# Performance work log

Hardware: AMD Instinct MI355X
Metric: run time of the kernel (lower is better)

## Reference

```python
import jax, jax.numpy as jnp
import numpy as np

HIDDEN = 4096
N_HEADS = 32
N_KV_HEADS = 8
HEAD_DIM = HIDDEN // N_HEADS  # 128
N_GROUPS = N_HEADS // N_KV_HEADS  # 4
MAX_POS = 4096
B, S = 2, 2048


def _rope_tables(max_pos, dim):
    # Mirrors create_sinusoidal_positions: freqs [pos, dim/2] -> emb [pos, dim]
    freqs = np.einsum('i,j->ij', np.arange(max_pos),
                      1.0 / 10000 ** (np.arange(0, dim, 2) / dim)).astype('float32')
    emb = np.concatenate((freqs, freqs), axis=-1)  # [pos, dim]
    return jnp.asarray(np.sin(emb)), jnp.asarray(np.cos(emb))

_SIN, _COS = _rope_tables(MAX_POS, HEAD_DIM)


def _apply_rope(t, sin_pos, cos_pos):
    # t: [B,S,H,hd]; sin/cos: [B,S,1,hd]
    half = t.shape[-1] // 2
    rot = jnp.concatenate((-t[..., half:], t[..., :half]), axis=-1)
    return t * cos_pos + rot * sin_pos


def setup_inputs() -> dict:
    key = jax.random.key(0)
    ks = jax.random.split(key, 5)
    std = 0.02
    hidden_states = jax.random.normal(ks[0], (B, S, HIDDEN), dtype=jnp.float32)
    attention_mask = jnp.ones((B, S), dtype=jnp.float32)
    position_ids = jnp.broadcast_to(jnp.arange(S, dtype=jnp.int32)[None, :], (B, S))
    Wq = jax.random.normal(ks[1], (HIDDEN, N_HEADS * HEAD_DIM), dtype=jnp.float32) * std
    Wk = jax.random.normal(ks[2], (HIDDEN, N_KV_HEADS * HEAD_DIM), dtype=jnp.float32) * std
    Wv = jax.random.normal(ks[3], (HIDDEN, N_KV_HEADS * HEAD_DIM), dtype=jnp.float32) * std
    Wo = jax.random.normal(ks[4], (HIDDEN, HIDDEN), dtype=jnp.float32) * std
    return {'hidden_states': hidden_states, 'attention_mask': attention_mask,
            'position_ids': position_ids, 'Wq': Wq, 'Wk': Wk, 'Wv': Wv, 'Wo': Wo}


def reference(hidden_states, attention_mask, position_ids, Wq, Wk, Wv, Wo):
    b, s, _ = hidden_states.shape
    # QKV projections (no bias) + head split
    q = (hidden_states @ Wq).reshape(b, s, N_HEADS, HEAD_DIM)
    k = (hidden_states @ Wk).reshape(b, s, N_KV_HEADS, HEAD_DIM)
    v = (hidden_states @ Wv).reshape(b, s, N_KV_HEADS, HEAD_DIM)
    # Rotary embedding
    sin_pos = _SIN[position_ids][:, :, None, :]  # [B,S,1,hd]
    cos_pos = _COS[position_ids][:, :, None, :]
    q = _apply_rope(q, sin_pos, cos_pos)
    k = _apply_rope(k, sin_pos, cos_pos)
    # Repeat KV heads for grouped-query attention
    k = jnp.repeat(k, N_GROUPS, axis=2)  # [B,S,H,hd]
    v = jnp.repeat(v, N_GROUPS, axis=2)
    # Causal mask & padding mask -> additive bias
    causal = jnp.tril(jnp.ones((s, s), dtype=bool))[None, None]  # [1,1,S,S]
    pad = (attention_mask > 0)[:, None, None, :]                 # [B,1,1,S]
    mask = jnp.logical_and(causal, pad)
    neg = jnp.finfo(jnp.float32).min
    bias = jnp.where(mask, 0.0, neg).astype(jnp.float32)
    # Scaled dot-product attention (softmax in fp32, matching flax)
    scale = 1.0 / jnp.sqrt(jnp.asarray(HEAD_DIM, dtype=jnp.float32))
    scores = jnp.einsum('bqhd,bkhd->bhqk', q * scale, k) + bias
    attn = jax.nn.softmax(scores, axis=-1)
    out = jnp.einsum('bhqk,bkhd->bqhd', attn, v).reshape(b, s, HIDDEN)
    return out @ Wo
```

## Files before the change

kernel.cpp:

```cpp
#include <hip/hip_runtime.h>

typedef unsigned short u16;
typedef __attribute__((ext_vector_type(8))) short bf16x8;
typedef __attribute__((ext_vector_type(8))) unsigned short u16x8;
typedef __attribute__((ext_vector_type(4))) float f32x4;

#define HIDDEN 4096
#define NH 32
#define NKV 8
#define HD 128
#define BB 2
#define SS 2048
#define TOK (BB * SS)
#define MAXPOS 4096
#define NQKV 6144

__device__ __forceinline__ u16 f2bf(float f) {
  unsigned u = __float_as_uint(f);
  u += 0x7FFFu + ((u >> 16) & 1u);
  return (u16)(u >> 16);
}
__device__ __forceinline__ float bf2f(u16 u) {
  return __uint_as_float(((unsigned)u) << 16);
}

__device__ __forceinline__ void gload_lds16(const u16* g, u16* l) {
  __builtin_amdgcn_global_load_lds(
      (const __attribute__((address_space(1))) unsigned int*)g,
      (__attribute__((address_space(3))) unsigned int*)l, 16, 0, 0);
}

__device__ __forceinline__ u16* swzp(u16* base, int row, int col, int stride) {
  int off = (row * stride + col) * 2;
  off ^= (row & 7) << 4;
  return (u16*)((char*)base + off);
}
__device__ __forceinline__ const u16* swzc(const u16* base, int row, int col, int stride) {
  int off = (row * stride + col) * 2;
  off ^= (row & 7) << 4;
  return (const u16*)((const char*)base + off);
}


__global__ void conv_bf16(const float* __restrict__ X, u16* __restrict__ Y, int n8) {
  int i = blockIdx.x * 256 + threadIdx.x;
  if (i >= n8) return;
  const float4* p = (const float4*)X;
  float4 a = p[2 * (long)i], b = p[2 * (long)i + 1];
  u16x8 o;
  o[0] = f2bf(a.x); o[1] = f2bf(a.y); o[2] = f2bf(a.z); o[3] = f2bf(a.w);
  o[4] = f2bf(b.x); o[5] = f2bf(b.y); o[6] = f2bf(b.z); o[7] = f2bf(b.w);
  *(u16x8*)&Y[(long)i * 8] = o;
}

__global__ __launch_bounds__(256) void conv_transpose(const float* __restrict__ W,
                                                      u16* __restrict__ Wt,
                                                      int K, int N) {
  __shared__ float tile[64][65];
  const int n0 = blockIdx.x * 64, k0 = blockIdx.y * 64;
  const int t = threadIdx.x;
  const int r = t >> 4, c4 = (t & 15) * 4;
#pragma unroll
  for (int i = 0; i < 4; i++) {
    float4 v = *(const float4*)&W[(long)(k0 + r + i * 16) * N + n0 + c4];
    tile[r + i * 16][c4 + 0] = v.x;
    tile[r + i * 16][c4 + 1] = v.y;
    tile[r + i * 16][c4 + 2] = v.z;
    tile[r + i * 16][c4 + 3] = v.w;
  }
  __syncthreads();
#pragma unroll
  for (int i = 0; i < 4; i++) {
    int n = r + i * 16;
    ushort4 o;
    o.x = f2bf(tile[c4 + 0][n]);
    o.y = f2bf(tile[c4 + 1][n]);
    o.z = f2bf(tile[c4 + 2][n]);
    o.w = f2bf(tile[c4 + 3][n]);
    *(ushort4*)&Wt[(long)(n0 + n) * K + k0 + c4] = o;
  }
}


__global__ void rope_table(float* __restrict__ st, float* __restrict__ ct) {
  int i = blockIdx.x * 256 + threadIdx.x;
  int pos = i >> 6, j = i & 63;
  float inv = exp2f(-(float)(2 * j) * (13.287712379549449f / 128.f));
  float a = (float)pos * inv;
  st[i] = sinf(a);
  ct[i] = cosf(a);
}

__global__ void rope_apply(u16* __restrict__ T, const int* __restrict__ pid,
                           const float* __restrict__ st, const float* __restrict__ ct,
                           int nh, int total, float scale) {
  int i = blockIdx.x * 256 + threadIdx.x;
  if (i >= total) return;
  int j = i & 63;
  int rest = i >> 6;
  int h = rest % nh;
  int tok = rest / nh;
  int pos = pid[tok];
  long base = ((long)tok * nh + h) * 128;
  float c = ct[pos * 64 + j], s = st[pos * 64 + j];
  float a = bf2f(T[base + j]), b = bf2f(T[base + 64 + j]);
  T[base + j]      = f2bf((a * c - b * s) * scale);
  T[base + 64 + j] = f2bf((b * c + a * s) * scale);
}

__global__ void mask_flags(const float* __restrict__ amask, int* __restrict__ mf) {
  int i = threadIdx.x;
  if (i >= BB * (SS / 64)) return;
  int b = i / (SS / 64), tt = i % (SS / 64);
  int any = 0;
  for (int k = 0; k < 64; k++) any |= (amask[b * SS + tt * 64 + k] <= 0.f) ? 1 : 0;
  mf[i] = any;
}

__global__ __launch_bounds__(256) void vtrans(const u16* __restrict__ V, u16* __restrict__ Vt) {
  __shared__ u16 tile[64][68];
  const int s0 = blockIdx.x * 64, d0 = blockIdx.y * 64;
  const int bk = blockIdx.z;
  const int b = bk >> 3, kvh = bk & 7;
  const int t = threadIdx.x;
  const int r = t >> 4, c4 = (t & 15) * 4;
#pragma unroll
  for (int i = 0; i < 4; i++) {
    int s = s0 + r + i * 16;
    ushort4 v = *(const ushort4*)&V[(((long)b * SS + s) * NKV + kvh) * HD + d0 + c4];
    tile[r + i * 16][c4 + 0] = v.x;
    tile[r + i * 16][c4 + 1] = v.y;
    tile[r + i * 16][c4 + 2] = v.z;
    tile[r + i * 16][c4 + 3] = v.w;
  }
  __syncthreads();
#pragma unroll
  for (int i = 0; i < 4; i++) {
    int d = r + i * 16;
    ushort4 o;
    o.x = tile[c4 + 0][d];
    o.y = tile[c4 + 1][d];
    o.z = tile[c4 + 2][d];
    o.w = tile[c4 + 3][d];
    *(ushort4*)&Vt[(((long)bk) * HD + d0 + d) * SS + s0 + c4] = o;
  }
}


#define GEMM256_CORE(Aptr, Btptr, Kd)                                              \
  __shared__ __align__(16) u16 ring[65536];       \
  const int tid = threadIdx.x;                                                     \
  const int lane = tid & 63;                                                       \
  const int wid = tid >> 6;                                                        \
  const int wm = wid >> 2, wn = wid & 3;                                           \
  const int fr = lane & 15, fq = lane >> 4;                                        \
  const int sr = tid >> 2;                                 \
  const int ss = (tid & 3) ^ ((sr ^ (sr >> 2)) & 3);        \
  const int csl = (fq ^ ((fr ^ (fr >> 2)) & 3)) << 4;      \
  const u16* Ag0 = (Aptr) + (brow + sr) * (long)(Kd) + ss * 8;                     \
  const u16* Bg0 = (Btptr) + (bcol + sr) * (long)(Kd) + ss * 8;                    \
  f32x4 acc[8][4] = {};                                                            \
  auto stage = [&](int tt) {                                                       \
    u16* as_ = &ring[(tt & 3) * 16384];                                            \
    const u16* ag = Ag0 + (long)tt * 32;                                           \
    const u16* bg = Bg0 + (long)tt * 32;                                           \
    gload_lds16(ag, as_ + tid * 8);                                                \
    gload_lds16(ag + 128 * (long)(Kd), as_ + 4096 + tid * 8);                      \
    gload_lds16(bg, as_ + 8192 + tid * 8);                                         \
    gload_lds16(bg + 128 * (long)(Kd), as_ + 12288 + tid * 8);                     \
  };                                                                               \
  const int NT = (Kd) / 32;                                                        \
  stage(0); stage(1); stage(2);                                                    \
  _Pragma("unroll 1")                                                              \
  for (int t = 0; t < NT; ++t) {                                                   \
    if (t + 2 < NT)      asm volatile("s_waitcnt vmcnt(8)" ::: "memory");          \
    else if (t + 1 < NT) asm volatile("s_waitcnt vmcnt(4)" ::: "memory");          \
    else                 asm volatile("s_waitcnt vmcnt(0)" ::: "memory");          \
    __builtin_amdgcn_s_barrier();                                                  \
    __builtin_amdgcn_sched_barrier(0);                                             \
    if (t + 3 < NT) stage(t + 3);      \
    const u16* as_ = &ring[(t & 3) * 16384];                                       \
    bf16x8 af[8], bfv[4];                                                          \
    _Pragma("unroll") for (int m = 0; m < 8; m++)                                  \
      af[m] = *(const bf16x8*)((const char*)as_ +                                  \
                               ((wm * 128 + m * 16 + fr) << 6) + csl);             \
    _Pragma("unroll") for (int n = 0; n < 4; n++)                                  \
      bfv[n] = *(const bf16x8*)((const char*)as_ + 16384 +                         \
                                ((wn * 64 + n * 16 + fr) << 6) + csl);             \
    asm volatile("s_waitcnt lgkmcnt(0)" ::: "memory");                             \
    __builtin_amdgcn_sched_barrier(0);                                             \
    __builtin_amdgcn_s_setprio(1);                                                 \
    _Pragma("unroll") for (int m = 0; m < 8; m++)                                  \
      _Pragma("unroll") for (int n = 0; n < 4; n++)                                \
        acc[m][n] = __builtin_amdgcn_mfma_f32_16x16x32_bf16(af[m], bfv[n],         \
                                                            acc[m][n], 0, 0, 0);   \
    __builtin_amdgcn_s_setprio(0);                                                 \
  }

#define XCD_BLOCK_MAP()                                                            \
  const int nwg = gridDim.x * gridDim.y;                                           \
  int bid = blockIdx.y * gridDim.x + blockIdx.x;                                   \
  bid = (bid & 7) * (nwg >> 3) + (bid >> 3);                                       \
  const long brow = (long)(bid / gridDim.x) * 256;                                 \
  const long bcol = (long)(bid % gridDim.x) * 256;

__global__ __launch_bounds__(512) void gemm_qkv(const u16* __restrict__ A,
                                                const u16* __restrict__ Bt,
                                                u16* __restrict__ Qb,
                                                u16* __restrict__ Kb,
                                                u16* __restrict__ Vb) {
  XCD_BLOCK_MAP()
  GEMM256_CORE(A, Bt, HIDDEN)
  u16* dst;
  long nst, cb;
  if (bcol < 4096)      { dst = Qb; nst = 4096; cb = bcol; }
  else if (bcol < 5120) { dst = Kb; nst = 1024; cb = bcol - 4096; }
  else                  { dst = Vb; nst = 1024; cb = bcol - 5120; }
#pragma unroll
  for (int m = 0; m < 8; m++)
#pragma unroll
    for (int j = 0; j < 4; j++) {
      long row = brow + wm * 128 + m * 16 + fq * 4 + j;
#pragma unroll
      for (int n = 0; n < 4; n++)
        dst[row * nst + cb + wn * 64 + n * 16 + fr] = f2bf(acc[m][n][j]);
    }
}

__global__ __launch_bounds__(512) void gemm_out(const u16* __restrict__ A,
                                                const u16* __restrict__ Bt,
                                                float* __restrict__ C) {
  XCD_BLOCK_MAP()
  GEMM256_CORE(A, Bt, HIDDEN)
#pragma unroll
  for (int m = 0; m < 8; m++)
#pragma unroll
    for (int j = 0; j < 4; j++) {
      long row = brow + wm * 128 + m * 16 + fq * 4 + j;
#pragma unroll
      for (int n = 0; n < 4; n++)
        C[row * HIDDEN + bcol + wn * 64 + n * 16 + fr] = acc[m][n][j];
    }
}


__global__ __launch_bounds__(256) void attn_fwd(const u16* __restrict__ Q,
                                                const u16* __restrict__ K,
                                                const u16* __restrict__ Vt,
                                                const float* __restrict__ amask,
                                                const int* __restrict__ mflag,
                                                u16* __restrict__ O) {
  const int b = blockIdx.z, h = blockIdx.y;
  const int qi = gridDim.x - 1 - blockIdx.x;
  const int qb = qi * 64;
  const int kvh = h >> 2;
  const int t = threadIdx.x, lane = t & 63, w = t >> 6;
  const int fr = lane & 15, fq = lane >> 4;

  __shared__ u16 Kl[2][64 * 128];
  __shared__ u16 Vl[2][128 * 64];
  __shared__ u16 PlA[4][16 * 64];

  const int qrow = qb + w * 16 + fr;
  bf16x8 qf[4];
  {
    const long qbase = (((long)b * SS + qrow) * NH + h) * HD;
#pragma unroll
    for (int kk = 0; kk < 4; kk++)
      qf[kk] = *(const bf16x8*)&Q[qbase + kk * 32 + fq * 8];
  }

  const u16* Kh = K + (long)b * SS * NKV * HD + (long)kvh * HD;
  const u16* Vh = Vt + ((long)b * NKV + kvh) * (long)HD * SS;
  const float* Mh = amask + (long)b * SS;
  const int* Mf = mflag + b * (SS / 64);
  u16* Plw = PlA[w];

  int koff[4], voff[4];
#pragma unroll
  for (int i = 0; i < 4; i++) {
    int o = i * 4096 + t * 16;
    int rk = o >> 8;
    int ck = (o & 255) ^ ((rk & 7) << 4);
    koff[i] = rk * (NKV * HD) + (ck >> 1);
    int rv = o >> 7;
    int cv = (o & 127) ^ ((rv & 7) << 4);
    voff[i] = rv * SS + (cv >> 1);
  }
  auto stage = [&](int kv0, int buf) {
    const u16* Kt = Kh + (long)kv0 * (NKV * HD);
    const u16* Vs = Vh + kv0;
#pragma unroll
    for (int i = 0; i < 4; i++)
      gload_lds16(Kt + koff[i], &Kl[buf][i * 2048 + t * 8]);
#pragma unroll
    for (int i = 0; i < 4; i++)
      gload_lds16(Vs + voff[i], &Vl[buf][i * 2048 + t * 8]);
  };

  f32x4 oacc[8] = {};
  float mrow = -1e30f, lrow = 0.f;
  const float L2E = 1.4426950408889634f;
  const int nt = qi + 1;

  stage(0, 0);

  for (int kvt = 0; kvt < nt; kvt++) {
    const int cur = kvt & 1;
    const int kv0 = kvt * 64;

    __syncthreads();
    if (kvt + 1 < nt) stage(kv0 + 64, cur ^ 1);
    __builtin_amdgcn_sched_barrier(0);

    f32x4 sacc[4] = {};
    __builtin_amdgcn_s_setprio(1);
#pragma unroll
    for (int n = 0; n < 4; n++)
#pragma unroll
      for (int kk = 0; kk < 4; kk++) {
        bf16x8 kf = *(const bf16x8*)swzc(&Kl[cur][0], n * 16 + fr, kk * 32 + fq * 8, 128);
        sacc[n] = __builtin_amdgcn_mfma_f32_16x16x32_bf16(kf, qf[kk], sacc[n], 0, 0, 0);
      }
    __builtin_amdgcn_s_setprio(0);

    if (kvt == qi) {
#pragma unroll
      for (int n = 0; n < 4; n++)
#pragma unroll
        for (int j = 0; j < 4; j++) {
          const int key = kv0 + n * 16 + fq * 4 + j;
          if (key > qrow) sacc[n][j] = -1e30f;
        }
    }
    if (Mf[kvt]) {
#pragma unroll
      for (int n = 0; n < 4; n++) {
        float4 mkv = *(const float4*)&Mh[kv0 + n * 16 + fq * 4];
#pragma unroll
        for (int j = 0; j < 4; j++)
          if ((&mkv.x)[j] <= 0.f) sacc[n][j] = -1e30f;
      }
    }

    float mn[4];
#pragma unroll
    for (int n = 0; n < 4; n++)
      mn[n] = fmaxf(fmaxf(sacc[n][0], sacc[n][1]), fmaxf(sacc[n][2], sacc[n][3]));
    float mx = fmaxf(fmaxf(mn[0], mn[1]), fmaxf(mn[2], mn[3]));
    mx = fmaxf(mx, __shfl_xor(mx, 16, 64));
    mx = fmaxf(mx, __shfl_xor(mx, 32, 64));

    if (__any(mx > mrow + 8.f)) {
      float mnew = fmaxf(mrow, mx);
      float alpha = exp2f((mrow - mnew) * L2E);
      lrow *= alpha;
      mrow = mnew;
      float aj[4];
#pragma unroll
      for (int j = 0; j < 4; j++) aj[j] = __shfl(alpha, fq * 4 + j, 64);
#pragma unroll
      for (int no = 0; no < 8; no++)
#pragma unroll
        for (int j = 0; j < 4; j++) oacc[no][j] *= aj[j];
    }

    float sn[4];
#pragma unroll
    for (int n = 0; n < 4; n++) {
#pragma unroll
      for (int j = 0; j < 4; j++)
        sacc[n][j] = exp2f((sacc[n][j] - mrow) * L2E);
      sn[n] = (sacc[n][0] + sacc[n][1]) + (sacc[n][2] + sacc[n][3]);
    }
    float sum = (sn[0] + sn[1]) + (sn[2] + sn[3]);
    sum += __shfl_xor(sum, 16, 64);
    sum += __shfl_xor(sum, 32, 64);
    lrow += sum;

#pragma unroll
    for (int n = 0; n < 4; n++) {
      ushort4 pw;
      pw.x = f2bf(sacc[n][0]);
      pw.y = f2bf(sacc[n][1]);
      pw.z = f2bf(sacc[n][2]);
      pw.w = f2bf(sacc[n][3]);
      *(ushort4*)swzp(Plw, fr, n * 16 + fq * 4, 64) = pw;
    }

    __builtin_amdgcn_s_setprio(1);
#pragma unroll
    for (int kk = 0; kk < 2; kk++) {
      bf16x8 pf = *(const bf16x8*)swzc(Plw, fr, kk * 32 + fq * 8, 64);
#pragma unroll
      for (int no = 0; no < 8; no++) {
        bf16x8 vf = *(const bf16x8*)swzc(&Vl[cur][0], no * 16 + fr, kk * 32 + fq * 8, 64);
        oacc[no] = __builtin_amdgcn_mfma_f32_16x16x32_bf16(pf, vf, oacc[no], 0, 0, 0);
      }
    }
    __builtin_amdgcn_s_setprio(0);
  }

  float lj[4];
#pragma unroll
  for (int j = 0; j < 4; j++) lj[j] = __shfl(lrow, fq * 4 + j, 64);
#pragma unroll
  for (int j = 0; j < 4; j++) {
    const int row = qb + w * 16 + fq * 4 + j;
    const float inv = 1.0f / lj[j];
    const long obase = (((long)b * SS + row) * NH + h) * HD;
#pragma unroll
    for (int no = 0; no < 8; no++)
      O[obase + no * 16 + fr] = f2bf(oacc[no][j] * inv);
  }
}


extern "C" void kernel_launch(void* const* d_in, const int* in_sizes, int n_in,
                              void* d_out, int out_size, void* d_ws, size_t ws_size,
                              hipStream_t stream) {
  const float* hs    = (const float*)d_in[0];
  const float* amask = (const float*)d_in[1];
  const int*   pid   = (const int*)d_in[2];
  const float* Wq    = (const float*)d_in[3];
  const float* Wk    = (const float*)d_in[4];
  const float* Wv    = (const float*)d_in[5];
  const float* Wo    = (const float*)d_in[6];
  float* out = (float*)d_out;

  char* ws = (char*)d_ws;
  const size_t MB = 1024ull * 1024ull;
  u16* Xb    = (u16*)(ws + 0);
  u16* Wqkvt = (u16*)(ws + 32 * MB);
  u16* Wot   = (u16*)(ws + 80 * MB);
  u16* Qb    = (u16*)(ws + 112 * MB);
  u16* Kb    = (u16*)(ws + 144 * MB);
  u16* Vb    = (u16*)(ws + 152 * MB);
  u16* Vtb   = (u16*)(ws + 160 * MB);
  float* st  = (float*)(ws + 168 * MB);
  float* ct  = (float*)(ws + 169 * MB);
  int* mf    = (int*)(ws + 170 * MB);
  u16* Ab = Xb;

  rope_table<<<(MAXPOS * 64) / 256, 256, 0, stream>>>(st, ct);
  mask_flags<<<1, 64, 0, stream>>>(amask, mf);
  conv_bf16<<<(TOK * HIDDEN / 8) / 256, 256, 0, stream>>>(hs, Xb, TOK * HIDDEN / 8);
  conv_transpose<<<dim3(HIDDEN / 64, HIDDEN / 64), 256, 0, stream>>>(Wq, Wqkvt, HIDDEN, HIDDEN);
  conv_transpose<<<dim3(1024 / 64, HIDDEN / 64), 256, 0, stream>>>(Wk, Wqkvt + 4096ull * 4096, HIDDEN, 1024);
  conv_transpose<<<dim3(1024 / 64, HIDDEN / 64), 256, 0, stream>>>(Wv, Wqkvt + 5120ull * 4096, HIDDEN, 1024);
  conv_transpose<<<dim3(HIDDEN / 64, HIDDEN / 64), 256, 0, stream>>>(Wo, Wot, HIDDEN, HIDDEN);

  gemm_qkv<<<dim3(NQKV / 256, TOK / 256), 512, 0, stream>>>(Xb, Wqkvt, Qb, Kb, Vb);

  const float qscale = 0.08838834764831845f;
  rope_apply<<<(TOK * NH * 64) / 256, 256, 0, stream>>>(Qb, pid, st, ct, NH, TOK * NH * 64, qscale);
  rope_apply<<<(TOK * NKV * 64) / 256, 256, 0, stream>>>(Kb, pid, st, ct, NKV, TOK * NKV * 64, 1.0f);

  vtrans<<<dim3(SS / 64, HD / 64, BB * NKV), 256, 0, stream>>>(Vb, Vtb);

  attn_fwd<<<dim3(SS / 64, NH, BB), 256, 0, stream>>>(Qb, Kb, Vtb, amask, mf, Ab);

  gemm_out<<<dim3(HIDDEN / 256, TOK / 256), 512, 0, stream>>>(Ab, Wot, out);
}
```

Before: 749.0 us.

## Vectorize RoPE kernel, use HIP bf16 conversion, drop explicit LDS wait in GEMM loop

The RoPE apply kernel now processes four elements per thread, using float4 loads of the sin/cos tables and ushort4 loads and stores of the bf16 data, with a quarter of the threads. The manual round-to-nearest bf16 conversion is replaced by the HIP intrinsic __float2bfloat16. The explicit lgkmcnt(0) wait and sched_barrier before the MFMA block in the GEMM main loop are removed, letting the compiler insert waits and interleave LDS reads with MFMAs. The changes target memory-op count and instruction overhead in the small elementwise kernel, and scheduling freedom in the GEMMs, at the risk of worse compiler scheduling in the GEMM loop.

```diff
diff --git a/kernel.cpp b/kernel.cpp
--- a/kernel.cpp
+++ b/kernel.cpp
@@ -1,4 +1,5 @@
 #include <hip/hip_runtime.h>
+#include <hip/hip_bf16.h>
 
 typedef unsigned short u16;
 typedef __attribute__((ext_vector_type(8))) short bf16x8;
@@ -16,9 +17,10 @@
 #define NQKV 6144
 
 __device__ __forceinline__ u16 f2bf(float f) {
-  unsigned u = __float_as_uint(f);
-  u += 0x7FFFu + ((u >> 16) & 1u);
-  return (u16)(u >> 16);
+  __hip_bfloat16 h = __float2bfloat16(f);
+  union { __hip_bfloat16 h; u16 u; } cv;
+  cv.h = h;
+  return cv.u;
 }
 __device__ __forceinline__ float bf2f(u16 u) {
   return __uint_as_float(((unsigned)u) << 16);
@@ -93,19 +95,42 @@
 
 __global__ void rope_apply(u16* __restrict__ T, const int* __restrict__ pid,
                            const float* __restrict__ st, const float* __restrict__ ct,
-                           int nh, int total, float scale) {
+                           int nh, int total4, float scale) {
   int i = blockIdx.x * 256 + threadIdx.x;
-  if (i >= total) return;
-  int j = i & 63;
-  int rest = i >> 6;
+  if (i >= total4) return;
+  int j4 = (i & 15) * 4;
+  int rest = i >> 4;
   int h = rest % nh;
   int tok = rest / nh;
   int pos = pid[tok];
   long base = ((long)tok * nh + h) * 128;
-  float c = ct[pos * 64 + j], s = st[pos * 64 + j];
-  float a = bf2f(T[base + j]), b = bf2f(T[base + 64 + j]);
-  T[base + j]      = f2bf((a * c - b * s) * scale);
-  T[base + 64 + j] = f2bf((b * c + a * s) * scale);
+  float4 c = *(const float4*)&ct[pos * 64 + j4];
+  float4 s = *(const float4*)&st[pos * 64 + j4];
+  ushort4 a4 = *(const ushort4*)&T[base + j4];
+  ushort4 b4 = *(const ushort4*)&T[base + 64 + j4];
+  ushort4 ra, rb;
+  {
+    float a = bf2f(a4.x), b = bf2f(b4.x);
+    ra.x = f2bf((a * c.x - b * s.x) * scale);
+    rb.x = f2bf((b * c.x + a * s.x) * scale);
+  }
+  {
+    float a = bf2f(a4.y), b = bf2f(b4.y);
+    ra.y = f2bf((a * c.y - b * s.y) * scale);
+    rb.y = f2bf((b * c.y + a * s.y) * scale);
+  }
+  {
+    float a = bf2f(a4.z), b = bf2f(b4.z);
+    ra.z = f2bf((a * c.z - b * s.z) * scale);
+    rb.z = f2bf((b * c.z + a * s.z) * scale);
+  }
+  {
+    float a = bf2f(a4.w), b = bf2f(b4.w);
+    ra.w = f2bf((a * c.w - b * s.w) * scale);
+    rb.w = f2bf((b * c.w + a * s.w) * scale);
+  }
+  *(ushort4*)&T[base + j4] = ra;
+  *(ushort4*)&T[base + 64 + j4] = rb;
 }
 
 __global__ void mask_flags(const float* __restrict__ amask, int* __restrict__ mf) {
@@ -187,8 +212,6 @@
     _Pragma("unroll") for (int n = 0; n < 4; n++)                                  \
       bfv[n] = *(const bf16x8*)((const char*)as_ + 16384 +                         \
                                 ((wn * 64 + n * 16 + fr) << 6) + csl);             \
-    asm volatile("s_waitcnt lgkmcnt(0)" ::: "memory");                             \
-    __builtin_amdgcn_sched_barrier(0);                                             \
     __builtin_amdgcn_s_setprio(1);                                                 \
     _Pragma("unroll") for (int m = 0; m < 8; m++)                                  \
       _Pragma("unroll") for (int n = 0; n < 4; n++)                                \
@@ -453,8 +476,8 @@
   gemm_qkv<<<dim3(NQKV / 256, TOK / 256), 512, 0, stream>>>(Xb, Wqkvt, Qb, Kb, Vb);
 
   const float qscale = 0.08838834764831845f;
-  rope_apply<<<(TOK * NH * 64) / 256, 256, 0, stream>>>(Qb, pid, st, ct, NH, TOK * NH * 64, qscale);
-  rope_apply<<<(TOK * NKV * 64) / 256, 256, 0, stream>>>(Kb, pid, st, ct, NKV, TOK * NKV * 64, 1.0f);
+  rope_apply<<<(TOK * NH * 16) / 256, 256, 0, stream>>>(Qb, pid, st, ct, NH, TOK * NH * 16, qscale);
+  rope_apply<<<(TOK * NKV * 16) / 256, 256, 0, stream>>>(Kb, pid, st, ct, NKV, TOK * NKV * 16, 1.0f);
 
   vtrans<<<dim3(SS / 64, HD / 64, BB * NKV), 256, 0, stream>>>(Vb, Vtb);
 
```

Result: faster. 719.5 us (-3.9%).
